# Optimization experiments

Hardware: AMD Instinct MI355X
Metric: run time of the kernel (lower is better)

## Reference

```python
import jax, jax.numpy as jnp
import numpy as np

NUM_QUBITS = 4
NUM_LAYERS = 3
C64 = jnp.complex64


def _apply_1q(state, U, axis):
    """Apply a single-qubit gate. state: (M,2,2,2,2); U: (2,2) shared or (M,2,2) per-batch."""
    s = jnp.moveaxis(state, axis, -1)
    if U.ndim == 2:
        s = jnp.einsum('...b,ab->...a', s, U)
    else:
        s = jnp.einsum('m...b,mab->m...a', s, U)
    return jnp.moveaxis(s, -1, axis)


def _apply_cnot(state, c_axis, t_axis):
    """CNOT: flip target amplitudes where control bit == 1."""
    s0 = jax.lax.index_in_dim(state, 0, axis=c_axis, keepdims=True)
    s1 = jax.lax.index_in_dim(state, 1, axis=c_axis, keepdims=True)
    s1 = jnp.flip(s1, axis=t_axis)
    return jnp.concatenate([s0, s1], axis=c_axis)


def _rx_mat(theta):
    """theta: (M,) -> (M,2,2) RX matrices."""
    c = jnp.cos(theta / 2).astype(C64)
    s = (-1j * jnp.sin(theta / 2)).astype(C64)
    row0 = jnp.stack([c, s], axis=-1)
    row1 = jnp.stack([s, c], axis=-1)
    return jnp.stack([row0, row1], axis=-2)


def _rot_mat(phi, theta, omega):
    """PennyLane Rot(phi,theta,omega) = RZ(omega) RY(theta) RZ(phi) -> (2,2)."""
    c = jnp.cos(theta / 2).astype(C64)
    s = jnp.sin(theta / 2).astype(C64)
    m00 = jnp.exp(-0.5j * (phi + omega).astype(C64)) * c
    m01 = -jnp.exp(0.5j * (phi - omega).astype(C64)) * s
    m10 = jnp.exp(-0.5j * (phi - omega).astype(C64)) * s
    m11 = jnp.exp(0.5j * (phi + omega).astype(C64)) * c
    return jnp.stack([jnp.stack([m00, m01]), jnp.stack([m10, m11])])


def setup_inputs() -> dict:
    key = jax.random.key(0)
    k1, k2 = jax.random.split(key)
    x = jax.random.normal(k1, (256, 4096, 4), dtype=jnp.float32)
    params = jax.random.normal(k2, (NUM_LAYERS, NUM_QUBITS, 3), dtype=jnp.float32) * 0.1
    return {"x": x, "params": params}


def reference(x, params):
    B, N, _ = x.shape
    M = B * N
    angles = x.reshape(M, NUM_QUBITS)

    # |0000> initial state, batched: (M, 2,2,2,2)
    state = jnp.zeros((M, 16), dtype=C64).at[:, 0].set(1.0)
    state = state.reshape((M,) + (2,) * NUM_QUBITS)

    # data-encoding RX layer (per-patch angles)
    for q in range(NUM_QUBITS):
        state = _apply_1q(state, _rx_mat(angles[:, q]), 1 + q)

    # variational layers: Rot on every qubit, then CNOT chain
    for l in range(NUM_LAYERS):
        for q in range(NUM_QUBITS):
            U = _rot_mat(params[l, q, 0], params[l, q, 1], params[l, q, 2])
            state = _apply_1q(state, U, 1 + q)
        for q in range(NUM_QUBITS - 1):
            state = _apply_cnot(state, 1 + q, 2 + q)

    # <Z_q> = P(bit_q=0) - P(bit_q=1)
    probs = state.real ** 2 + state.imag ** 2  # (M,2,2,2,2)
    zs = []
    for q in range(NUM_QUBITS):
        p = jnp.moveaxis(probs, 1 + q, 1)
        zs.append(jnp.sum(p[:, 0] - p[:, 1], axis=(1, 2, 3)))
    return jnp.stack(zs, axis=-1).reshape(B, N, NUM_QUBITS)
```

## Files before the change

### kernel.cpp

```cpp
#include <hip/hip_runtime.h>

__global__ __launch_bounds__(256) void qprecomp(const float* __restrict__ params,
                                                float* __restrict__ C) {
  __shared__ float colR[16][16];
  __shared__ float colI[16][16];
  __shared__ float Um[12][8];
  __shared__ float4 S4[256];
  const int t = threadIdx.x;

  if (t < 16) {
#pragma unroll
    for (int i = 0; i < 16; ++i) { colR[t][i] = 0.0f; colI[t][i] = 0.0f; }
    int pc = __popc(t) & 3;
    colR[t][t] = (pc == 0) ? 1.0f : (pc == 2 ? -1.0f : 0.0f);
    colI[t][t] = (pc == 1) ? -1.0f : (pc == 3 ? 1.0f : 0.0f);
  }
  if (t < 12) {
    float phi = params[t * 3 + 0], th = params[t * 3 + 1], om = params[t * 3 + 2];
    float sa = __sinf(0.5f * (phi + om)), ca = __cosf(0.5f * (phi + om));
    float sb = __sinf(0.5f * (phi - om)), cb = __cosf(0.5f * (phi - om));
    float s2 = __sinf(0.5f * th),         c2 = __cosf(0.5f * th);
    Um[t][0] =  c2 * ca; Um[t][1] = -c2 * sa;
    Um[t][2] = -s2 * cb; Um[t][3] = -s2 * sb;
    Um[t][4] =  s2 * cb; Um[t][5] = -s2 * sb;
    Um[t][6] =  c2 * ca; Um[t][7] =  c2 * sa;
  }
  __syncthreads();

  const int j = t >> 3, p = t & 7;
  for (int l = 0; l < 3; ++l) {
    for (int q = 0; q < 4; ++q) {
      if (t < 128) {
        const int g = l * 4 + q;
        const int B = 3 - q, mask = 1 << B;
        const int i0 = ((p >> B) << (B + 1)) | (p & (mask - 1));
        const int i1 = i0 | mask;
        float a0r = colR[j][i0], a0i = colI[j][i0];
        float a1r = colR[j][i1], a1i = colI[j][i1];
        float m00r = Um[g][0], m00i = Um[g][1], m01r = Um[g][2], m01i = Um[g][3];
        float m10r = Um[g][4], m10i = Um[g][5], m11r = Um[g][6], m11i = Um[g][7];
        colR[j][i0] = m00r * a0r - m00i * a0i + m01r * a1r - m01i * a1i;
        colI[j][i0] = m00r * a0i + m00i * a0r + m01r * a1i + m01i * a1r;
        colR[j][i1] = m10r * a0r - m10i * a0i + m11r * a1r - m11i * a1i;
        colI[j][i1] = m10r * a0i + m10i * a0r + m11r * a1i + m11i * a1r;
      }
      __syncthreads();
    }
    for (int q = 0; q < 3; ++q) {
      if (t < 64) {
        const int jj = t >> 2, pp = t & 3;
        const int Bc = 3 - q, Bt = 2 - q;
        int fps[2], nf = 0;
        for (int b = 0; b < 4; ++b)
          if (b != Bc && b != Bt) fps[nf++] = b;
        const int i  = (1 << Bc) | ((pp & 1) << fps[0]) | (((pp >> 1) & 1) << fps[1]);
        const int i2 = i | (1 << Bt);
        float tr = colR[jj][i], ti = colI[jj][i];
        colR[jj][i] = colR[jj][i2]; colI[jj][i] = colI[jj][i2];
        colR[jj][i2] = tr;          colI[jj][i2] = ti;
      }
      __syncthreads();
    }
  }

  {
    const int jj = t >> 4, k = t & 15;
    float s0 = 0.f, s1 = 0.f, s2 = 0.f, s3 = 0.f;
#pragma unroll
    for (int i = 0; i < 16; ++i) {
      float pr = colR[jj][i] * colR[k][i] + colI[jj][i] * colI[k][i];
      s0 += ((i >> 3) & 1) ? -pr : pr;
      s1 += ((i >> 2) & 1) ? -pr : pr;
      s2 += ((i >> 1) & 1) ? -pr : pr;
      s3 += ( i       & 1) ? -pr : pr;
    }
    S4[t] = make_float4(s0, s1, s2, s3);
  }
  __syncthreads();

  if (t < 81) {
    const int m[4] = { t / 27, (t / 9) % 3, (t / 3) % 3, t % 3 };
    float a0 = 0.f, a1 = 0.f, a2 = 0.f, a3 = 0.f;
    for (int c = 0; c < 16; ++c) {
      int jj = 0, kk = 0; bool ok = true;
      for (int q = 0; q < 4; ++q) {
        int jb, kb;
        if (m[q] == 1) { jb = (c >> q) & 1; kb = 1 - jb; }
        else { jb = kb = (m[q] >> 1); if ((c >> q) & 1) ok = false; }
        jj |= jb << (3 - q); kk |= kb << (3 - q);
      }
      if (!ok) continue;
      float4 sv = S4[jj * 16 + kk];
      a0 += sv.x; a1 += sv.y; a2 += sv.z; a3 += sv.w;
    }
    C[t * 4 + 0] = a0 * 0.0625f;
    C[t * 4 + 1] = a1 * 0.0625f;
    C[t * 4 + 2] = a2 * 0.0625f;
    C[t * 4 + 3] = a3 * 0.0625f;
  }
}

__device__ __forceinline__ void build_t(const float4 a, float* t01, float* t23) {
  const float s0 = __sinf(a.x), c0 = __cosf(a.x);
  const float s1 = __sinf(a.y), c1 = __cosf(a.y);
  const float s2 = __sinf(a.z), c2 = __cosf(a.z);
  const float s3 = __sinf(a.w), c3 = __cosf(a.w);
  float w0[3] = { 1.0f + c0, s0, 1.0f - c0 };
  float w1[3] = { 1.0f + c1, s1, 1.0f - c1 };
  float w2[3] = { 1.0f + c2, s2, 1.0f - c2 };
  float w3[3] = { 1.0f + c3, s3, 1.0f - c3 };
#pragma unroll
  for (int i = 0; i < 3; ++i)
#pragma unroll
    for (int jj = 0; jj < 3; ++jj) {
      t01[i * 3 + jj] = w0[i] * w1[jj];
      t23[i * 3 + jj] = w2[i] * w3[jj];
    }
}

__global__ __launch_bounds__(256) void qmain(const float4* __restrict__ x4,
                                             const float4* __restrict__ C4,
                                             float4* __restrict__ out,
                                             int half) {
  const int gid = blockIdx.x * 256 + threadIdx.x;
  float tA01[9], tA23[9], tB01[9], tB23[9];
  build_t(x4[gid], tA01, tA23);
  build_t(x4[gid + half], tB01, tB23);

  float2 accA01 = make_float2(0.f, 0.f), accA23 = make_float2(0.f, 0.f);
  float2 accB01 = make_float2(0.f, 0.f), accB23 = make_float2(0.f, 0.f);
#pragma unroll
  for (int a = 0; a < 9; ++a) {
#pragma unroll
    for (int b = 0; b < 9; ++b) {
      const float4 c = C4[a * 9 + b];
      const float2 c01 = make_float2(c.x, c.y);
      const float2 c23 = make_float2(c.z, c.w);
      const float pA = tA01[a] * tA23[b];
      const float pB = tB01[a] * tB23[b];
      const float2 pA2 = make_float2(pA, pA);
      const float2 pB2 = make_float2(pB, pB);
      accA01 = make_float2(fmaf(c01.x, pA2.x, accA01.x), fmaf(c01.y, pA2.y, accA01.y));
      accA23 = make_float2(fmaf(c23.x, pA2.x, accA23.x), fmaf(c23.y, pA2.y, accA23.y));
      accB01 = make_float2(fmaf(c01.x, pB2.x, accB01.x), fmaf(c01.y, pB2.y, accB01.y));
      accB23 = make_float2(fmaf(c23.x, pB2.x, accB23.x), fmaf(c23.y, pB2.y, accB23.y));
    }
  }
  out[gid]        = make_float4(accA01.x, accA01.y, accA23.x, accA23.y);
  out[gid + half] = make_float4(accB01.x, accB01.y, accB23.x, accB23.y);
}

extern "C" void kernel_launch(void* const* d_in, const int* in_sizes, int n_in,
                              void* d_out, int out_size, void* d_ws, size_t ws_size,
                              hipStream_t stream) {
  const float* x      = (const float*)d_in[0];
  const float* params = (const float*)d_in[1];
  float* C = (float*)d_ws;

  qprecomp<<<1, 256, 0, stream>>>(params, C);

  const int M    = in_sizes[0] / 4;
  const int half = M / 2;
  const int blocks = half / 256;
  qmain<<<blocks, 256, 0, stream>>>((const float4*)x, (const float4*)C,
                                    (float4*)d_out, half);
}
```

Before: 23.17 us.

## Factor 9x9 contraction, stage coefficients in LDS, process four elements per thread

Rewrites the main contraction as a two-level sum: an inner sum over b using t23 coefficients, then one multiply by t01[a]. This drops the per-term product tA01*tA23. The 81 coefficient float4s are now staged in shared memory. Each thread handles four elements instead of two, amortising coefficient loads, at the cost of more registers, half as many blocks, and a non-unrolled outer loop.

Result: slower. 34.86 us (+50.4%).

```diff
diff --git a/kernel.cpp b/kernel.cpp
--- a/kernel.cpp
+++ b/kernel.cpp
@@ -100,54 +100,83 @@
   }
 }
 
-__device__ __forceinline__ void build_t(const float4 a, float* t01, float* t23) {
+struct TF { float t01[9]; float t23[9]; };
+
+__device__ __forceinline__ void build_t(const float4 a, TF& tf) {
   const float s0 = __sinf(a.x), c0 = __cosf(a.x);
   const float s1 = __sinf(a.y), c1 = __cosf(a.y);
   const float s2 = __sinf(a.z), c2 = __cosf(a.z);
   const float s3 = __sinf(a.w), c3 = __cosf(a.w);
-  float w0[3] = { 1.0f + c0, s0, 1.0f - c0 };
-  float w1[3] = { 1.0f + c1, s1, 1.0f - c1 };
-  float w2[3] = { 1.0f + c2, s2, 1.0f - c2 };
-  float w3[3] = { 1.0f + c3, s3, 1.0f - c3 };
+  const float w0[3] = { 1.0f + c0, s0, 1.0f - c0 };
+  const float w1[3] = { 1.0f + c1, s1, 1.0f - c1 };
+  const float w2[3] = { 1.0f + c2, s2, 1.0f - c2 };
+  const float w3[3] = { 1.0f + c3, s3, 1.0f - c3 };
 #pragma unroll
   for (int i = 0; i < 3; ++i)
 #pragma unroll
     for (int jj = 0; jj < 3; ++jj) {
-      t01[i * 3 + jj] = w0[i] * w1[jj];
-      t23[i * 3 + jj] = w2[i] * w3[jj];
+      tf.t01[i * 3 + jj] = w0[i] * w1[jj];
+      tf.t23[i * 3 + jj] = w2[i] * w3[jj];
     }
 }
 
 __global__ __launch_bounds__(256) void qmain(const float4* __restrict__ x4,
                                              const float4* __restrict__ C4,
                                              float4* __restrict__ out,
-                                             int half) {
-  const int gid = blockIdx.x * 256 + threadIdx.x;
-  float tA01[9], tA23[9], tB01[9], tB23[9];
-  build_t(x4[gid], tA01, tA23);
-  build_t(x4[gid + half], tB01, tB23);
+                                             int quarter) {
+  __shared__ float4 Cs[81];
+  const int t = threadIdx.x;
+  if (t < 81) Cs[t] = C4[t];
 
-  float2 accA01 = make_float2(0.f, 0.f), accA23 = make_float2(0.f, 0.f);
-  float2 accB01 = make_float2(0.f, 0.f), accB23 = make_float2(0.f, 0.f);
+  const int gid = blockIdx.x * 256 + t;
+  TF tf[4];
+  build_t(x4[gid],               tf[0]);
+  build_t(x4[gid + quarter],     tf[1]);
+  build_t(x4[gid + 2 * quarter], tf[2]);
+  build_t(x4[gid + 3 * quarter], tf[3]);
+  __syncthreads();
+
+  float2 z01[4], z23[4];
 #pragma unroll
+  for (int e = 0; e < 4; ++e) {
+    z01[e] = make_float2(0.f, 0.f);
+    z23[e] = make_float2(0.f, 0.f);
+  }
+
+#pragma unroll 1
   for (int a = 0; a < 9; ++a) {
+    float2 v01[4], v23[4];
+#pragma unroll
+    for (int e = 0; e < 4; ++e) {
+      v01[e] = make_float2(0.f, 0.f);
+      v23[e] = make_float2(0.f, 0.f);
+    }
 #pragma unroll
     for (int b = 0; b < 9; ++b) {
-      const float4 c = C4[a * 9 + b];
-      const float2 c01 = make_float2(c.x, c.y);
-      const float2 c23 = make_float2(c.z, c.w);
-      const float pA = tA01[a] * tA23[b];
-      const float pB = tB01[a] * tB23[b];
-      const float2 pA2 = make_float2(pA, pA);
-      const float2 pB2 = make_float2(pB, pB);
-      accA01 = make_float2(fmaf(c01.x, pA2.x, accA01.x), fmaf(c01.y, pA2.y, accA01.y));
-      accA23 = make_float2(fmaf(c23.x, pA2.x, accA23.x), fmaf(c23.y, pA2.y, accA23.y));
-      accB01 = make_float2(fmaf(c01.x, pB2.x, accB01.x), fmaf(c01.y, pB2.y, accB01.y));
-      accB23 = make_float2(fmaf(c23.x, pB2.x, accB23.x), fmaf(c23.y, pB2.y, accB23.y));
+      const float4 c = Cs[a * 9 + b];
+#pragma unroll
+      for (int e = 0; e < 4; ++e) {
+        const float tb = tf[e].t23[b];
+        v01[e].x = fmaf(c.x, tb, v01[e].x);
+        v01[e].y = fmaf(c.y, tb, v01[e].y);
+        v23[e].x = fmaf(c.z, tb, v23[e].x);
+        v23[e].y = fmaf(c.w, tb, v23[e].y);
+      }
+    }
+#pragma unroll
+    for (int e = 0; e < 4; ++e) {
+      const float ta = tf[e].t01[a];
+      z01[e].x = fmaf(ta, v01[e].x, z01[e].x);
+      z01[e].y = fmaf(ta, v01[e].y, z01[e].y);
+      z23[e].x = fmaf(ta, v23[e].x, z23[e].x);
+      z23[e].y = fmaf(ta, v23[e].y, z23[e].y);
     }
   }
-  out[gid]        = make_float4(accA01.x, accA01.y, accA23.x, accA23.y);
-  out[gid + half] = make_float4(accB01.x, accB01.y, accB23.x, accB23.y);
+
+  out[gid]               = make_float4(z01[0].x, z01[0].y, z23[0].x, z23[0].y);
+  out[gid + quarter]     = make_float4(z01[1].x, z01[1].y, z23[1].x, z23[1].y);
+  out[gid + 2 * quarter] = make_float4(z01[2].x, z01[2].y, z23[2].x, z23[2].y);
+  out[gid + 3 * quarter] = make_float4(z01[3].x, z01[3].y, z23[3].x, z23[3].y);
 }
 
 extern "C" void kernel_launch(void* const* d_in, const int* in_sizes, int n_in,
@@ -159,9 +188,9 @@
 
   qprecomp<<<1, 256, 0, stream>>>(params, C);
 
-  const int M    = in_sizes[0] / 4;
-  const int half = M / 2;
-  const int blocks = half / 256;
+  const int M       = in_sizes[0] / 4;
+  const int quarter = M / 4;
+  const int blocks  = quarter / 256;
   qmain<<<blocks, 256, 0, stream>>>((const float4*)x, (const float4*)C,
-                                    (float4*)d_out, half);
+                                    (float4*)d_out, quarter);
 }
```
